# Kernel optimization log

Hardware: AMD Instinct MI355X
Metric: run time of the kernel (lower is better)

## Reference

```python
import jax, jax.numpy as jnp
import numpy as np

H = 8192   # lattice vertex count (all levels, synthetic, == hash_cnt)
N0 = 8192  # output point count
F = 15     # permutohedral filter size: (t+1)^(d+1) - t^(d+1), t=1, d=3
NEG = 0.1  # LeakyReLU negative slope

def lrelu(x):
    return jnp.where(x >= 0, x, NEG * x)

def conv1x1(x, w, b):
    # x (B,C,N), w (O,C), b (O,)
    return jnp.einsum('oc,bcn->bon', w, x) + b[None, :, None]

def splat(feat, bary, offset, num):
    # barycentric scatter of point features onto lattice: (B,C,N)->(B,C,num)
    w = feat[:, :, None, :] * bary[:, None, :, :]  # (B,C,4,N)
    def one(wb, ob):
        C = wb.shape[0]
        return jax.ops.segment_sum(wb.reshape(C, -1).T, ob.reshape(-1), num_segments=num).T
    return jax.vmap(one)(w, offset)

def gather(lat, idx):
    # lat (B,C,H), idx (B,K,N) -> (B,C,K,N)
    return jax.vmap(lambda f, i: f[:, i])(lat, idx)

def slice_lat(lat, bary, offset):
    # barycentric interpolation from lattice back to points: (B,C,N)
    return jnp.einsum('bcjn,bjn->bcn', gather(lat, offset), bary)

def blur_mlp(lat, nbrs, w0, b0, w1, b1):
    # BilateralConvFlex blur: gather F lattice neighbors, 1x1-conv MLP (last_relu=False)
    g = gather(lat, nbrs)  # (B,C,F,H)
    B, C, Fk, Hk = g.shape
    h = lrelu(conv1x1(g.reshape(B, C * Fk, Hk), w0, b0))
    return conv1x1(h, w1, b1)

def corr_block(feat1_pts, feat2_lat, prev_pts, bary1, off1, out_bary, out_off,
               idx1, idx2, wc0, bc0, wc1, bc1, wo0, bo0, wo1, bo1):
    # BilateralCorrelationFlex: splat pc1, hash-indexed patch correlation with pc2
    # lattice, per-displacement corr MLP, flatten over displacements, out MLP, slice.
    L1 = splat(feat1_pts, bary1, off1, H)                  # (B,C,H)
    x = gather(L1, idx1) * gather(feat2_lat, idx2)         # (B,C,F,H)
    if prev_pts is not None:
        P1 = splat(prev_pts, bary1, off1, H)
        x = jnp.concatenate([x, gather(P1, idx1)], axis=1)
    h = lrelu(jnp.einsum('oc,bcfh->bofh', wc0, x) + bc0[None, :, None, None])
    h = lrelu(jnp.einsum('oc,bcfh->bofh', wc1, h) + bc1[None, :, None, None])
    B, Co, Fk, Hk = h.shape
    h = lrelu(conv1x1(h.reshape(B, Co * Fk, Hk), wo0, bo0))
    h = conv1x1(h, wo1, bo1)                               # last_relu=False
    return slice_lat(h, out_bary, out_off)

def setup_inputs():
    key = jax.random.key(0)
    ks = iter(jax.random.split(key, 100))
    def randn(shape):
        return jax.random.normal(next(ks), shape, dtype=jnp.float32)
    def bary(n):
        b = jax.random.uniform(next(ks), (1, 4, n), dtype=jnp.float32)
        return b / jnp.sum(b, axis=1, keepdims=True)
    def ridx(shape, hi):
        return jax.random.randint(next(ks), shape, 0, hi)
    def W(o, c):
        return jax.random.normal(next(ks), (o, c), dtype=jnp.float32) / np.float32(np.sqrt(c))
    def bias(o):
        return jax.random.normal(next(ks), (o,), dtype=jnp.float32) * 0.01
    inp = {}
    for n in ['feat0_1', 'feat0_2', 'feat0_4', 'feat1_1', 'feat1_2', 'feat1_4']:
        inp[n] = randn((1, 32, H))
    for n in ['g2_pc1_el_minus_gr', 'g2_pc2_el_minus_gr', 'g1_pc1_el_minus_gr', 'g1_pc2_el_minus_gr']:
        inp[n] = randn((1, 4, H))
    inp['g2_pc1_barycentric'] = bary(H); inp['g2_pc2_barycentric'] = bary(H)
    inp['g1_pc1_barycentric'] = bary(H); inp['g1_pc2_barycentric'] = bary(H)
    inp['g0_pc1_barycentric'] = bary(N0)
    for n in ['g2_pc1_lattice_offset', 'g2_pc2_lattice_offset', 'g1_pc1_lattice_offset', 'g1_pc2_lattice_offset']:
        inp[n] = ridx((1, 4, H), H)
    inp['g0_pc1_lattice_offset'] = ridx((1, 4, N0), H)
    for n in ['g1_pc1_blur_neighbors', 'g1_pc2_blur_neighbors', 'g0_pc1_blur_neighbors', 'g0_pc2_blur_neighbors',
              'g1_pc1_corr_indices', 'g1_pc2_corr_indices', 'g0_pc1_corr_indices', 'g0_pc2_corr_indices']:
        inp[n] = ridx((1, F, H), H)
    inp['w_embed2'] = W(128, 32); inp['b_embed2'] = bias(128)
    inp['w_embed1'] = W(256, 32); inp['b_embed1'] = bias(256)
    inp['w_up2_0'] = W(256, 132 * F); inp['b_up2_0'] = bias(256)
    inp['w_up2_1'] = W(256, 256); inp['b_up2_1'] = bias(256)
    inp['w_up1_0'] = W(512, 516 * F); inp['b_up1_0'] = bias(512)
    inp['w_up1_1'] = W(512, 512); inp['b_up1_1'] = bias(512)
    inp['w_c2_corr0'] = W(32, 256); inp['b_c2_corr0'] = bias(32)
    inp['w_c2_corr1'] = W(32, 32); inp['b_c2_corr1'] = bias(32)
    inp['w_c2_out0'] = W(256, 32 * F); inp['b_c2_out0'] = bias(256)
    inp['w_c2_out1'] = W(256, 256); inp['b_c2_out1'] = bias(256)
    inp['w_c1_corr0'] = W(32, 512 + 256); inp['b_c1_corr0'] = bias(32)
    inp['w_c1_corr1'] = W(32, 32); inp['b_c1_corr1'] = bias(32)
    inp['w_c1_out0'] = W(512, 32 * F); inp['b_c1_out0'] = bias(512)
    inp['w_c1_out1'] = W(512, 512); inp['b_c1_out1'] = bias(512)
    inp['w_s4'] = W(512, 512); inp['b_s4'] = bias(512)
    inp['w_s2'] = W(256, 512); inp['b_s2'] = bias(256)
    inp['w_s1'] = W(3, 256); inp['b_s1'] = bias(3)
    return inp

def reference(feat0_1, feat0_2, feat0_4, feat1_1, feat1_2, feat1_4,
              g2_pc1_el_minus_gr, g2_pc2_el_minus_gr, g1_pc1_el_minus_gr, g1_pc2_el_minus_gr,
              g2_pc1_barycentric, g2_pc2_barycentric, g1_pc1_barycentric, g1_pc2_barycentric, g0_pc1_barycentric,
              g2_pc1_lattice_offset, g2_pc2_lattice_offset, g1_pc1_lattice_offset, g1_pc2_lattice_offset, g0_pc1_lattice_offset,
              g1_pc1_blur_neighbors, g1_pc2_blur_neighbors, g0_pc1_blur_neighbors, g0_pc2_blur_neighbors,
              g1_pc1_corr_indices, g1_pc2_corr_indices, g0_pc1_corr_indices, g0_pc2_corr_indices,
              w_embed2, b_embed2, w_embed1, b_embed1,
              w_up2_0, b_up2_0, w_up2_1, b_up2_1, w_up1_0, b_up1_0, w_up1_1, b_up1_1,
              w_c2_corr0, b_c2_corr0, w_c2_corr1, b_c2_corr1, w_c2_out0, b_c2_out0, w_c2_out1, b_c2_out1,
              w_c1_corr0, b_c1_corr0, w_c1_corr1, b_c1_corr1, w_c1_out0, b_c1_out0, w_c1_out1, b_c1_out1,
              w_s4, b_s4, w_s2, b_s2, w_s1, b_s1):
    # conv4_embed and feat*_4 are defined but unused in the original forward.
    f0_2 = lrelu(conv1x1(feat0_2, w_embed2, b_embed2))
    f1_2 = lrelu(conv1x1(feat1_2, w_embed2, b_embed2))
    blur0 = blur_mlp(jnp.concatenate([g2_pc1_el_minus_gr, f0_2], axis=1),
                     g1_pc1_blur_neighbors, w_up2_0, b_up2_0, w_up2_1, b_up2_1)
    pcl0_2 = slice_lat(blur0, g2_pc1_barycentric, g2_pc1_lattice_offset)
    pcl0_2_to_1 = slice_lat(blur0, g1_pc1_barycentric, g1_pc1_lattice_offset)
    blur1 = blur_mlp(jnp.concatenate([g2_pc2_el_minus_gr, f1_2], axis=1),
                     g1_pc2_blur_neighbors, w_up2_0, b_up2_0, w_up2_1, b_up2_1)
    pcl1_2 = slice_lat(blur1, g2_pc2_barycentric, g2_pc2_lattice_offset)
    pcl1_2_to_1 = slice_lat(blur1, g1_pc2_barycentric, g1_pc2_lattice_offset)
    corr2 = corr_block(pcl0_2, pcl1_2, None, g2_pc1_barycentric, g2_pc1_lattice_offset,
                       g1_pc1_barycentric, g1_pc1_lattice_offset,
                       g1_pc1_corr_indices, g1_pc2_corr_indices,
                       w_c2_corr0, b_c2_corr0, w_c2_corr1, b_c2_corr1,
                       w_c2_out0, b_c2_out0, w_c2_out1, b_c2_out1)
    f0_1 = lrelu(conv1x1(feat0_1, w_embed1, b_embed1))
    f1_1 = lrelu(conv1x1(feat1_1, w_embed1, b_embed1))
    lat0 = blur_mlp(jnp.concatenate([g1_pc1_el_minus_gr, pcl0_2_to_1, f0_1], axis=1),
                    g0_pc1_blur_neighbors, w_up1_0, b_up1_0, w_up1_1, b_up1_1)
    pcl0_1 = slice_lat(lat0, g1_pc1_barycentric, g1_pc1_lattice_offset)
    lat1 = blur_mlp(jnp.concatenate([g1_pc2_el_minus_gr, pcl1_2_to_1, f1_1], axis=1),
                    g0_pc2_blur_neighbors, w_up1_0, b_up1_0, w_up1_1, b_up1_1)
    pcl1_1 = slice_lat(lat1, g1_pc2_barycentric, g1_pc2_lattice_offset)
    corr1 = corr_block(pcl0_1, pcl1_1, corr2, g1_pc1_barycentric, g1_pc1_lattice_offset,
                       g0_pc1_barycentric, g0_pc1_lattice_offset,
                       g0_pc1_corr_indices, g0_pc2_corr_indices,
                       w_c1_corr0, b_c1_corr0, w_c1_corr1, b_c1_corr1,
                       w_c1_out0, b_c1_out0, w_c1_out1, b_c1_out1)
    res = lrelu(conv1x1(corr1, w_s4, b_s4))
    res = lrelu(conv1x1(res, w_s2, b_s2))
    return conv1x1(res, w_s1, b_s1)  # (1, 3, N0)
```

## Files before the change

kernel.cpp:

```cpp
#include <hip/hip_runtime.h>
#include <hip/hip_bf16.h>

#define HDIM 8192
#define FK 15

typedef __attribute__((ext_vector_type(8))) short bf16x8;
typedef __attribute__((ext_vector_type(4))) float f32x4;

__device__ __forceinline__ void gload_lds16(const void* g, void* l) {
    __builtin_amdgcn_global_load_lds(
        (const __attribute__((address_space(1))) void*)g,
        (__attribute__((address_space(3))) void*)l, 16, 0, 0);
}

__global__ void k_pack(const float* __restrict__ W, __hip_bfloat16* __restrict__ P,
                       int O, int C, int Cp, int Fk, int mode) {
    int e = blockIdx.x * 256 + threadIdx.x;
    int total = Fk * Cp * O;
    if (e >= total) return;
    int j = e & 7;
    int lane = (e >> 3) & 63;
    int tile = e >> 9;
    int OT = O >> 4;
    int ot = tile % OT, kt = tile / OT;
    int o = ot * 16 + (lane & 15);
    int kk = kt * 32 + (lane >> 4) * 8 + j;
    float v;
    if (mode == 1) {
        int f = kk / Cp, c = kk % Cp;
        v = (c < C) ? W[(size_t)o * C * Fk + (size_t)c * Fk + f] : 0.f;
    } else if (mode == 2) {
        int f = kk >> 5, oo = kk & 31;
        v = W[(size_t)o * 480 + oo * 15 + f];
    } else {
        v = W[(size_t)o * C + kk];
    }
    P[e] = __float2bfloat16(v);
}

__global__ void k_copy_el(const float* __restrict__ el, __hip_bfloat16* __restrict__ catT,
                          int N, int ld) {
    int n = blockIdx.x * 256 + threadIdx.x;
    if (n >= N) return;
#pragma unroll
    for (int j = 0; j < 4; ++j)
        catT[(size_t)n * ld + j] = __float2bfloat16(el[(size_t)j * N + n]);
}

__global__ __launch_bounds__(256) void k_embed(const float* __restrict__ X,
                                               const float* __restrict__ W,
                                               const float* __restrict__ b,
                                               __hip_bfloat16* __restrict__ outT,
                                               int N, int O, int ld, int coff) {
    __shared__ float Xs[32][65];
    int tid = threadIdx.x;
    int n0 = blockIdx.x * 64;
    for (int e = tid; e < 32 * 64; e += 256) {
        int nn = e & 63, c = e >> 6;
        Xs[c][nn] = X[(size_t)c * N + n0 + nn];
    }
    __syncthreads();
    int ol = tid & 63, nl = tid >> 6;
    for (int o0 = 0; o0 < O; o0 += 64) {
        int o = o0 + ol;
        float wv[32];
#pragma unroll
        for (int c = 0; c < 32; ++c) wv[c] = W[o * 32 + c];
        float bv = b[o];
        for (int nn = nl; nn < 64; nn += 4) {
            float acc = bv;
#pragma unroll
            for (int c = 0; c < 32; ++c) acc += wv[c] * Xs[c][nn];
            acc = acc >= 0.f ? acc : 0.1f * acc;
            outT[(size_t)(n0 + nn) * ld + coff + o] = __float2bfloat16(acc);
        }
    }
}

struct W4 { bf16x8 r0, r1, r2, r3; };

template<int OG, int HG, int MR>
__global__ __launch_bounds__(512, 2) void k_blur_fat(
    const __hip_bfloat16* __restrict__ A0b, const __hip_bfloat16* __restrict__ A1b,
    const int* __restrict__ n0, const int* __restrict__ n1,
    const __hip_bfloat16* __restrict__ Wb, float* __restrict__ hbuf,
    int Cp, int O, int H) {
    __shared__ short abuf[3 * 4096];
    __shared__ int idx_s[8 * 128];
    int z = blockIdx.z;
    int strm = z >> 1, kh = z & 1;
    const unsigned short* A = (const unsigned short*)(strm ? A1b : A0b);
    const int* nbrs = strm ? n1 : n0;
    int CpT = Cp >> 5, OT = O >> 4;
    int fbeg = kh ? 8 : 0;
    int fcnt = kh ? (FK - 8) : 8;
    int S = fcnt * CpT;
    float* outp = hbuf + (size_t)z * ((size_t)H * (size_t)O);
    const unsigned short* Wp = (const unsigned short*)Wb;
    int tid = threadIdx.x, lane = tid & 63, wid = tid >> 6;
    int r16 = lane & 15, g = lane >> 4;
    int og = (OG == 8) ? wid : (wid & 3);
    int hg = (OG == 8) ? 0 : (wid >> 2);
    int h0 = blockIdx.x * 128;
    int srow = tid >> 2;
    int sgseg = (tid & 3) ^ ((tid >> 3) & 3);
    int pseg = g ^ ((r16 >> 1) & 3);
    int hgbase = hg * (MR * 16);
    char* abase = (char*)abuf;

    for (int e = tid; e < fcnt * 128; e += 512)
        idx_s[e] = nbrs[(size_t)(fbeg + (e >> 7)) * H + h0 + (e & 127)];
    __syncthreads();

    f32x4 acc[MR][4];
#pragma unroll
    for (int m = 0; m < MR; ++m)
#pragma unroll
        for (int n = 0; n < 4; ++n) acc[m][n] = (f32x4){0.f, 0.f, 0.f, 0.f};

    W4 wA, wB, wC;
    int tS = 0, cS = 0, fS = 0;

#define STAGE_AW(SLOTA, W)                                                         \
    do {                                                                           \
        int gi = idx_s[fS * 128 + srow];                                           \
        gload_lds16(A + (size_t)gi * Cp + cS * 32 + sgseg * 8,                     \
                    abase + (SLOTA) * 8192 + wid * 1024);                          \
        const unsigned short* wbp =                                                \
            Wp + ((size_t)(((fbeg + fS) * CpT + cS) * OT + og * 4)) * 512 + lane * 8; \
        W.r0 = *(const bf16x8*)(wbp);                                              \
        W.r1 = *(const bf16x8*)(wbp + 512);                                        \
        W.r2 = *(const bf16x8*)(wbp + 1024);                                       \
        W.r3 = *(const bf16x8*)(wbp + 1536);                                       \
        if (tS < S - 1) { ++tS; if (++cS == CpT) { cS = 0; ++fS; } }               \
    } while (0)

#define FITER(SLOT, WCUR, WNXT)                                                    \
    do {                                                                           \
        __builtin_amdgcn_sched_barrier(0);                                         \
        asm volatile("s_waitcnt vmcnt(5)" ::: "memory");                           \
        __builtin_amdgcn_sched_barrier(0);                                         \
        __builtin_amdgcn_s_barrier();                                              \
        __builtin_amdgcn_sched_barrier(0);                                         \
        STAGE_AW(((SLOT) + 2) % 3, WNXT);                                          \
        const short* ab = abuf + (SLOT) * 4096;                                    \
        bf16x8 av[MR];                                                             \
        _Pragma("unroll")                                                          \
        for (int rb = 0; rb < MR; ++rb)                                            \
            av[rb] = *(const bf16x8*)(ab + (hgbase + rb * 16 + r16) * 32 + pseg * 8); \
        _Pragma("unroll")                                                          \
        for (int rb = 0; rb < MR; ++rb) {                                          \
            acc[rb][0] = __builtin_amdgcn_mfma_f32_16x16x32_bf16(av[rb], WCUR.r0, acc[rb][0], 0, 0, 0); \
            acc[rb][1] = __builtin_amdgcn_mfma_f32_16x16x32_bf16(av[rb], WCUR.r1, acc[rb][1], 0, 0, 0); \
            acc[rb][2] = __builtin_amdgcn_mfma_f32_16x16x32_bf16(av[rb], WCUR.r2, acc[rb][2], 0, 0, 0); \
            acc[rb][3] = __builtin_amdgcn_mfma_f32_16x16x32_bf16(av[rb], WCUR.r3, acc[rb][3], 0, 0, 0); \
        }                                                                          \
    } while (0)

    STAGE_AW(0, wA);
    STAGE_AW(1, wB);
    for (int t = 0; t < S; t += 3) {
        FITER(0, wA, wC);
        if (t + 1 < S) FITER(1, wB, wA);
        if (t + 2 < S) FITER(2, wC, wB);
    }
#undef FITER
#undef STAGE_AW

#pragma unroll
    for (int n = 0; n < 4; ++n) {
        int o = og * 64 + n * 16 + r16;
#pragma unroll
        for (int m = 0; m < MR; ++m)
#pragma unroll
            for (int i = 0; i < 4; ++i)
                outp[(size_t)(h0 + hgbase + m * 16 + g * 4 + i) * O + o] = acc[m][n][i];
    }
}

__global__ void k_comb(const float* __restrict__ p, const float* __restrict__ bias,
                       __hip_bfloat16* __restrict__ out, int NO, int Om) {
    int i = blockIdx.x * 256 + threadIdx.x;
    int stride = gridDim.x * 256;
    for (; i < NO; i += stride) {
        float v = p[i] + p[i + NO] + bias[i & Om];
        v = v >= 0.f ? v : 0.1f * v;
        out[i] = __float2bfloat16(v);
    }
}

#define DEF_PIPE_VARS                                                              \
    bf16x8 a00, a01, w00, w01, w02, w03;                                           \
    bf16x8 a10, a11, w10, w11, w12, w13;                                           \
    bf16x8 a20, a21, w20, w21, w22, w23;

#define LOADST(J, TEND, FEND)                                                      \
    do {                                                                           \
        const unsigned short* a0p = A + (size_t)i0c * Cp + cL * 32 + g * 8;        \
        const unsigned short* a1p = A + (size_t)i1c * Cp + cL * 32 + g * 8;        \
        a##J##0 = *(const bf16x8*)a0p;                                             \
        a##J##1 = *(const bf16x8*)a1p;                                             \
        const unsigned short* wbp = Wp + ((size_t)(tL * OT + otb)) * 512 + lane * 8; \
        w##J##0 = *(const bf16x8*)(wbp);                                           \
        w##J##1 = *(const bf16x8*)(wbp + 512);                                     \
        w##J##2 = *(const bf16x8*)(wbp + 1024);                                    \
        w##J##3 = *(const bf16x8*)(wbp + 1536);                                    \
        if (tL < (TEND) - 1) {                                                     \
            ++tL;                                                                  \
            if (++cL == CpT) {                                                     \
                cL = 0; ++fL;                                                      \
                i0c = i0n; i1c = i1n;                                              \
                if (fL + 1 < (FEND)) {                                             \
                    i0n = nbrs ? nbrs[(size_t)(fL + 1) * H + hrow] : hrow;         \
                    i1n = nbrs ? nbrs[(size_t)(fL + 1) * H + hrow + 16] : (hrow + 16); \
                }                                                                  \
            }                                                                      \
        }                                                                          \
    } while (0)

#define MFMAST(J)                                                                  \
    do {                                                                           \
        acc[0][0] = __builtin_amdgcn_mfma_f32_16x16x32_bf16(a##J##0, w##J##0, acc[0][0], 0, 0, 0); \
        acc[0][1] = __builtin_amdgcn_mfma_f32_16x16x32_bf16(a##J##0, w##J##1, acc[0][1], 0, 0, 0); \
        acc[0][2] = __builtin_amdgcn_mfma_f32_16x16x32_bf16(a##J##0, w##J##2, acc[0][2], 0, 0, 0); \
        acc[0][3] = __builtin_amdgcn_mfma_f32_16x16x32_bf16(a##J##0, w##J##3, acc[0][3], 0, 0, 0); \
        acc[1][0] = __builtin_amdgcn_mfma_f32_16x16x32_bf16(a##J##1, w##J##0, acc[1][0], 0, 0, 0); \
        acc[1][1] = __builtin_amdgcn_mfma_f32_16x16x32_bf16(a##J##1, w##J##1, acc[1][1], 0, 0, 0); \
        acc[1][2] = __builtin_amdgcn_mfma_f32_16x16x32_bf16(a##J##1, w##J##2, acc[1][2], 0, 0, 0); \
        acc[1][3] = __builtin_amdgcn_mfma_f32_16x16x32_bf16(a##J##1, w##J##3, acc[1][3], 0, 0, 0); \
    } while (0)

__global__ __launch_bounds__(256) void k_mfma_gemm(const __hip_bfloat16* __restrict__ Ab,
                                                   const int* __restrict__ nbrs,
                                                   const __hip_bfloat16* __restrict__ Wb,
                                                   const float* __restrict__ bias,
                                                   float* __restrict__ outF,
                                                   __hip_bfloat16* __restrict__ outB,
                                                   int Cp, int Fk, int O, int H, int act,
                                                   const __hip_bfloat16* Ab1,
                                                   float* outF1, __hip_bfloat16* outB1) {
    if (blockIdx.z) { Ab = Ab1; outF = outF1; outB = outB1; }
    const unsigned short* A = (const unsigned short*)Ab;
    const unsigned short* Wp = (const unsigned short*)Wb;
    int tid = threadIdx.x, lane = tid & 63, w = tid >> 6;
    int r16 = lane & 15, g = lane >> 4;
    int h0 = blockIdx.x * 128, o0 = blockIdx.y * 64;
    int OT = O >> 4, CpT = Cp >> 5, S = Fk * CpT;
    int otb = o0 >> 4;
    int w32 = w * 32;
    int hrow = h0 + w32 + r16;

    int i0c = nbrs ? nbrs[hrow] : hrow;
    int i1c = nbrs ? nbrs[hrow + 16] : (hrow + 16);
    int i0n = i0c, i1n = i1c;
    if (Fk > 1) {
        i0n = nbrs[(size_t)H + hrow];
        i1n = nbrs[(size_t)H + hrow + 16];
    }

    f32x4 acc[2][4];
#pragma unroll
    for (int m = 0; m < 2; ++m)
#pragma unroll
        for (int n = 0; n < 4; ++n) acc[m][n] = (f32x4){0.f, 0.f, 0.f, 0.f};

    DEF_PIPE_VARS
    int tL = 0, cL = 0, fL = 0;

    LOADST(0, S, Fk);
    LOADST(1, S, Fk);
    for (int sb = 0; sb < S; sb += 3) {
        LOADST(2, S, Fk);
        MFMAST(0);
        LOADST(0, S, Fk);
        if (sb + 1 < S) MFMAST(1);
        LOADST(1, S, Fk);
        if (sb + 2 < S) MFMAST(2);
    }

#pragma unroll
    for (int n = 0; n < 4; ++n) {
        int o = o0 + n * 16 + r16;
        float bv = bias[o];
#pragma unroll
        for (int m = 0; m < 2; ++m) {
#pragma unroll
            for (int i = 0; i < 4; ++i) {
                int h = h0 + w32 + m * 16 + g * 4 + i;
                float v = acc[m][n][i] + bv;
                if (act) v = v >= 0.f ? v : 0.1f * v;
                if (outF) outF[(size_t)h * O + o] = v;
                if (outB) outB[(size_t)h * O + o] = __float2bfloat16(v);
            }
        }
    }
}

__global__ void k_slice(const float* __restrict__ latT, const float* __restrict__ bary,
                        const int* __restrict__ off, float* __restrict__ outT,
                        int N, int C, int ld, int coff) {
    int cl = threadIdx.x & 63, rr = threadIdx.x >> 6;
    int n = blockIdx.x * 4 + rr;
    int c = blockIdx.y * 64 + cl;
    float s = 0.f;
#pragma unroll
    for (int j = 0; j < 4; ++j) {
        int o = off[(size_t)j * N + n];
        float w = bary[(size_t)j * N + n];
        s += latT[(size_t)o * C + c] * w;
    }
    outT[(size_t)n * ld + coff + c] = s;
}

__global__ void k_slice_b(const float* __restrict__ latT, const float* __restrict__ bary,
                          const int* __restrict__ off, __hip_bfloat16* __restrict__ outT,
                          int N, int C, int ld, int coff) {
    int cl = threadIdx.x & 63, rr = threadIdx.x >> 6;
    int n = blockIdx.x * 4 + rr;
    int c = blockIdx.y * 64 + cl;
    float s = 0.f;
#pragma unroll
    for (int j = 0; j < 4; ++j) {
        int o = off[(size_t)j * N + n];
        float w = bary[(size_t)j * N + n];
        s += latT[(size_t)o * C + c] * w;
    }
    outT[(size_t)n * ld + coff + c] = __float2bfloat16(s);
}

__global__ void k_splat(const float* __restrict__ featT, const float* __restrict__ bary,
                        const int* __restrict__ off, float* __restrict__ latT,
                        int N, int C) {
    int cl = threadIdx.x & 63, rr = threadIdx.x >> 6;
    int n = blockIdx.x * 4 + rr;
    int c = blockIdx.y * 64 + cl;
    float v = featT[(size_t)n * C + c];
#pragma unroll
    for (int j = 0; j < 4; ++j) {
        int o = off[(size_t)j * N + n];
        float w = bary[(size_t)j * N + n];
        atomicAdd(&latT[(size_t)o * C + c], v * w);
    }
}

__global__ __launch_bounds__(256) void k_corr_mfma(const float* __restrict__ L1T,
                                                   const float* __restrict__ f2T,
                                                   const float* __restrict__ P1T,
                                                   const int* __restrict__ idx1,
                                                   const int* __restrict__ idx2,
                                                   const __hip_bfloat16* __restrict__ W0p,
                                                   const float* __restrict__ b0,
                                                   const __hip_bfloat16* __restrict__ W1p,
                                                   const float* __restrict__ b1,
                                                   __hip_bfloat16* __restrict__ h1T,
                                                   int H, int C1, int C2) {
    __shared__ __hip_bfloat16 As[64 * 72];
    __shared__ __hip_bfloat16 A0s[64 * 40];
    __shared__ int i1s[64], i2s[64];
    int tid = threadIdx.x;
    int p0 = blockIdx.x * 64;
    int f = p0 >> 13;
    int h0 = p0 & (HDIM - 1);
    if (tid < 64) {
        i1s[tid] = idx1[(size_t)f * H + h0 + tid];
        i2s[tid] = idx2[(size_t)f * H + h0 + tid];
    }
    __syncthreads();
    int lane = tid & 63, wid = tid >> 6;
    int wh = wid * 16;
    int r16 = lane & 15, g = lane >> 4;
    int srow = tid >> 2, sseg = tid & 3;
    int K = C1 + C2;
    const unsigned short* W0u = (const unsigned short*)W0p;
    const unsigned short* W1u = (const unsigned short*)W1p;
    f32x4 acc[2];
    acc[0] = (f32x4){0.f, 0.f, 0.f, 0.f};
    acc[1] = (f32x4){0.f, 0.f, 0.f, 0.f};

    for (int c0 = 0; c0 < K; c0 += 64) {
        int cb = c0 + sseg * 16;
        float x[16];
        if (cb < C1) {
            const float4* a4 = (const float4*)(L1T + (size_t)i1s[srow] * C1 + cb);
            const float4* b4 = (const float4*)(f2T + (size_t)i2s[srow] * C1 + cb);
#pragma unroll
            for (int q = 0; q < 4; ++q) {
                float4 av = a4[q], bv = b4[q];
                x[q * 4 + 0] = av.x * bv.x; x[q * 4 + 1] = av.y * bv.y;
                x[q * 4 + 2] = av.z * bv.z; x[q * 4 + 3] = av.w * bv.w;
            }
        } else {
            const float4* a4 = (const float4*)(P1T + (size_t)i1s[srow] * C2 + (cb - C1));
#pragma unroll
            for (int q = 0; q < 4; ++q) {
                float4 av = a4[q];
                x[q * 4 + 0] = av.x; x[q * 4 + 1] = av.y;
                x[q * 4 + 2] = av.z; x[q * 4 + 3] = av.w;
            }
        }
        __syncthreads();
        __hip_bfloat16* dst = &As[srow * 72 + sseg * 16];
#pragma unroll
        for (int q = 0; q < 16; ++q) dst[q] = __float2bfloat16(x[q]);
        __syncthreads();
        int ktg = c0 >> 5;
#pragma unroll
        for (int kt = 0; kt < 2; ++kt) {
            bf16x8 a = *(const bf16x8*)(&As[(wh + r16) * 72 + kt * 32 + g * 8]);
            const unsigned short* wb = W0u + (size_t)((ktg + kt) * 2) * 512 + lane * 8;
            bf16x8 bf0 = *(const bf16x8*)(wb);
            bf16x8 bf1 = *(const bf16x8*)(wb + 512);
            acc[0] = __builtin_amdgcn_mfma_f32_16x16x32_bf16(a, bf0, acc[0], 0, 0, 0);
            acc[1] = __builtin_amdgcn_mfma_f32_16x16x32_bf16(a, bf1, acc[1], 0, 0, 0);
        }
    }
    __syncthreads();
#pragma unroll
    for (int ot = 0; ot < 2; ++ot) {
        int o = ot * 16 + r16;
        float bv = b0[o];
#pragma unroll
        for (int i = 0; i < 4; ++i) {
            int pr = wh + g * 4 + i;
            float v = acc[ot][i] + bv;
            v = v >= 0.f ? v : 0.1f * v;
            A0s[pr * 40 + o] = __float2bfloat16(v);
        }
    }
    __syncthreads();
    bf16x8 a1 = *(const bf16x8*)(&A0s[(wh + r16) * 40 + g * 8]);
    bf16x8 w1f0 = *(const bf16x8*)(W1u + lane * 8);
    bf16x8 w1f1 = *(const bf16x8*)(W1u + 512 + lane * 8);
    f32x4 acc1[2];
    acc1[0] = (f32x4){0.f, 0.f, 0.f, 0.f};
    acc1[1] = (f32x4){0.f, 0.f, 0.f, 0.f};
    acc1[0] = __builtin_amdgcn_mfma_f32_16x16x32_bf16(a1, w1f0, acc1[0], 0, 0, 0);
    acc1[1] = __builtin_amdgcn_mfma_f32_16x16x32_bf16(a1, w1f1, acc1[1], 0, 0, 0);
#pragma unroll
    for (int ot = 0; ot < 2; ++ot) {
        int o = ot * 16 + r16;
        float bv = b1[o];
#pragma unroll
        for (int i = 0; i < 4; ++i) {
            int h = h0 + wh + g * 4 + i;
            float v = acc1[ot][i] + bv;
            v = v >= 0.f ? v : 0.1f * v;
            h1T[(size_t)h * 480 + f * 32 + o] = __float2bfloat16(v);
        }
    }
}

__global__ void k_final(const float* __restrict__ r2T, const float* __restrict__ W,
                        const float* __restrict__ b, float* __restrict__ out, int N) {
    int n = blockIdx.x * 256 + threadIdx.x;
    if (n >= N) return;
    float s0 = b[0], s1 = b[1], s2 = b[2];
    const float4* x4 = (const float4*)(r2T + (size_t)n * 256);
    for (int q = 0; q < 64; ++q) {
        float4 v = x4[q];
        float xs[4] = {v.x, v.y, v.z, v.w};
#pragma unroll
        for (int u = 0; u < 4; ++u) {
            int c = 4 * q + u;
            s0 = fmaf(W[c], xs[u], s0);
            s1 = fmaf(W[256 + c], xs[u], s1);
            s2 = fmaf(W[512 + c], xs[u], s2);
        }
    }
    out[n] = s0;
    out[(size_t)N + n] = s1;
    out[(size_t)2 * N + n] = s2;
}

extern "C" void kernel_launch(void* const* d_in, const int* in_sizes, int n_in,
                              void* d_out, int out_size, void* d_ws, size_t ws_size,
                              hipStream_t stream) {
    const int N = HDIM;
    auto F32 = [&](int i) { return (const float*)d_in[i]; };
    auto I32 = [&](int i) { return (const int*)d_in[i]; };

    char* base = (char*)d_ws;
    size_t off = 0;
    auto allocB = [&](size_t elems) -> __hip_bfloat16* {
        __hip_bfloat16* r = (__hip_bfloat16*)(base + off);
        off += ((elems * 2 + 255) / 256) * 256;
        return r;
    };
    auto allocF = [&](size_t elems) -> float* {
        float* r = (float*)(base + off);
        off += ((elems * 4 + 255) / 256) * 256;
        return r;
    };

    __hip_bfloat16* pw_up2   = allocB((size_t)15 * 160 * 256);
    __hip_bfloat16* pw_up1   = allocB((size_t)15 * 544 * 512);
    __hip_bfloat16* pw_up2_1 = allocB((size_t)256 * 256);
    __hip_bfloat16* pw_up1_1 = allocB((size_t)512 * 512);
    __hip_bfloat16* pw_c2o   = allocB((size_t)480 * 256);
    __hip_bfloat16* pw_c2o1  = allocB((size_t)256 * 256);
    __hip_bfloat16* pw_c1o   = allocB((size_t)480 * 512);
    __hip_bfloat16* pw_c1o1  = allocB((size_t)512 * 512);
    __hip_bfloat16* pw_s4    = allocB((size_t)512 * 512);
    __hip_bfloat16* pw_s2    = allocB((size_t)512 * 256);
    __hip_bfloat16* pw_cc20  = allocB((size_t)256 * 32);
    __hip_bfloat16* pw_cc21  = allocB((size_t)32 * 32);
    __hip_bfloat16* pw_cc10  = allocB((size_t)768 * 32);
    __hip_bfloat16* pw_cc11  = allocB((size_t)32 * 32);
    __hip_bfloat16* catb2a = allocB((size_t)N * 160);
    __hip_bfloat16* catb2b = allocB((size_t)N * 160);
    __hip_bfloat16* catb1a = allocB((size_t)N * 544);
    __hip_bfloat16* catb1b = allocB((size_t)N * 544);
    __hip_bfloat16* ab512a = allocB((size_t)N * 512);
    __hip_bfloat16* ab512b = allocB((size_t)N * 512);
    __hip_bfloat16* ab256a = allocB((size_t)N * 256);
    __hip_bfloat16* ab256b = allocB((size_t)N * 256);
    __hip_bfloat16* h1b    = allocB((size_t)N * 480);
    __hip_bfloat16* corr1b = allocB((size_t)N * 512);
    float* T512a  = allocF((size_t)N * 512);
    float* T512b  = allocF((size_t)N * 512);
    float* pcl512 = allocF((size_t)N * 512);
    float* pcl01  = allocF((size_t)N * 512);
    float* pcl11  = allocF((size_t)N * 512);
    float* SL256  = allocF((size_t)N * 256);
    float* corr2T = allocF((size_t)N * 256);
    float* hbuf   = allocF((size_t)4 * N * 512);
    float* pclA = pcl512;
    float* pclB = pcl512 + (size_t)N * 256;
    float* SL512 = pcl512;
    float* SP256 = SL256;
    (void)ws_size; (void)in_sizes; (void)n_in; (void)out_size;

    auto pack = [&](const float* W, __hip_bfloat16* P, int O, int C, int Cp, int Fk, int mode) {
        int total = Fk * Cp * O;
        k_pack<<<(total + 255) / 256, 256, 0, stream>>>(W, P, O, C, Cp, Fk, mode);
    };
    pack(F32(32), pw_up2,   256, 132, 160, 15, 1);
    pack(F32(36), pw_up1,   512, 516, 544, 15, 1);
    pack(F32(34), pw_up2_1, 256, 256, 256, 1, 0);
    pack(F32(38), pw_up1_1, 512, 512, 512, 1, 0);
    pack(F32(44), pw_c2o,   256, 480, 480, 1, 2);
    pack(F32(46), pw_c2o1,  256, 256, 256, 1, 0);
    pack(F32(52), pw_c1o,   512, 480, 480, 1, 2);
    pack(F32(54), pw_c1o1,  512, 512, 512, 1, 0);
    pack(F32(56), pw_s4,    512, 512, 512, 1, 0);
    pack(F32(58), pw_s2,    256, 512, 512, 1, 0);
    pack(F32(40), pw_cc20,  32, 256, 256, 1, 0);
    pack(F32(42), pw_cc21,  32, 32, 32, 1, 0);
    pack(F32(48), pw_cc10,  32, 768, 768, 1, 0);
    pack(F32(50), pw_cc11,  32, 32, 32, 1, 0);

    hipMemsetAsync(catb2a, 0, (size_t)N * 160 * 2, stream);
    hipMemsetAsync(catb2b, 0, (size_t)N * 160 * 2, stream);
    hipMemsetAsync(catb1a, 0, (size_t)N * 544 * 2, stream);
    hipMemsetAsync(catb1b, 0, (size_t)N * 544 * 2, stream);
    hipMemsetAsync(SL256,  0, (size_t)N * 256 * 4, stream);

    k_copy_el<<<32, 256, 0, stream>>>(F32(6), catb2a, N, 160);
    k_embed<<<128, 256, 0, stream>>>(F32(1), F32(28), F32(29), catb2a, N, 128, 160, 4);
    k_copy_el<<<32, 256, 0, stream>>>(F32(7), catb2b, N, 160);
    k_embed<<<128, 256, 0, stream>>>(F32(4), F32(28), F32(29), catb2b, N, 128, 160, 4);
    k_blur_fat<4, 2, 4><<<dim3(64, 1, 4), 512, 0, stream>>>(catb2a, catb2b, I32(20), I32(21),
                                                            pw_up2, hbuf, 160, 256, N);
    k_comb<<<2048, 256, 0, stream>>>(hbuf, F32(33), ab256a, N * 256, 255);
    k_comb<<<2048, 256, 0, stream>>>(hbuf + (size_t)2 * N * 256, F32(33), ab256b, N * 256, 255);
    k_mfma_gemm<<<dim3(64, 4, 2), 256, 0, stream>>>(ab256a, nullptr, pw_up2_1, F32(35),
                                                    T512a, nullptr, 256, 1, 256, N, 0,
                                                    ab256b, T512b, nullptr);
    k_slice<<<dim3(2048, 4), 256, 0, stream>>>(T512a, F32(10), I32(15), pclA, N, 256, 256, 0);
    k_slice_b<<<dim3(2048, 4), 256, 0, stream>>>(T512a, F32(12), I32(17), catb1a, N, 256, 544, 4);
    k_slice<<<dim3(2048, 4), 256, 0, stream>>>(T512b, F32(11), I32(16), pclB, N, 256, 256, 0);
    k_slice_b<<<dim3(2048, 4), 256, 0, stream>>>(T512b, F32(13), I32(18), catb1b, N, 256, 544, 4);

    k_splat<<<dim3(2048, 4), 256, 0, stream>>>(pclA, F32(10), I32(15), SL256, N, 256);
    k_corr_mfma<<<FK * HDIM / 64, 256, 0, stream>>>(SL256, pclB, (const float*)nullptr,
                                                    I32(24), I32(25), pw_cc20, F32(41),
                                                    pw_cc21, F32(43), h1b, N, 256, 0);
    k_mfma_gemm<<<dim3(64, 4), 256, 0, stream>>>(h1b, nullptr, pw_c2o, F32(45),
                                                 nullptr, ab256a, 480, 1, 256, N, 1,
                                                 nullptr, nullptr, nullptr);
    k_mfma_gemm<<<dim3(64, 4), 256, 0, stream>>>(ab256a, nullptr, pw_c2o1, F32(47),
                                                 T512a, nullptr, 256, 1, 256, N, 0,
                                                 nullptr, nullptr, nullptr);
    k_slice<<<dim3(2048, 4), 256, 0, stream>>>(T512a, F32(12), I32(17), corr2T, N, 256, 256, 0);

    k_copy_el<<<32, 256, 0, stream>>>(F32(8), catb1a, N, 544);
    k_embed<<<128, 256, 0, stream>>>(F32(0), F32(30), F32(31), catb1a, N, 256, 544, 260);
    k_copy_el<<<32, 256, 0, stream>>>(F32(9), catb1b, N, 544);
    k_embed<<<128, 256, 0, stream>>>(F32(3), F32(30), F32(31), catb1b, N, 256, 544, 260);
    k_blur_fat<8, 1, 8><<<dim3(64, 1, 4), 512, 0, stream>>>(catb1a, catb1b, I32(22), I32(23),
                                                            pw_up1, hbuf, 544, 512, N);
    k_comb<<<2048, 256, 0, stream>>>(hbuf, F32(37), ab512a, N * 512, 511);
    k_comb<<<2048, 256, 0, stream>>>(hbuf + (size_t)2 * N * 512, F32(37), ab512b, N * 512, 511);
    k_mfma_gemm<<<dim3(64, 8, 2), 256, 0, stream>>>(ab512a, nullptr, pw_up1_1, F32(39),
                                                    T512a, nullptr, 512, 1, 512, N, 0,
                                                    ab512b, T512b, nullptr);
    k_slice<<<dim3(2048, 8), 256, 0, stream>>>(T512a, F32(12), I32(17), pcl01, N, 512, 512, 0);
    k_slice<<<dim3(2048, 8), 256, 0, stream>>>(T512b, F32(13), I32(18), pcl11, N, 512, 512, 0);

    hipMemsetAsync(SL512, 0, (size_t)N * 512 * 4, stream);
    k_splat<<<dim3(2048, 8), 256, 0, stream>>>(pcl01, F32(12), I32(17), SL512, N, 512);
    hipMemsetAsync(SP256, 0, (size_t)N * 256 * 4, stream);
    k_splat<<<dim3(2048, 4), 256, 0, stream>>>(corr2T, F32(12), I32(17), SP256, N, 256);
    k_corr_mfma<<<FK * HDIM / 64, 256, 0, stream>>>(SL512, pcl11, SP256,
                                                    I32(26), I32(27), pw_cc10, F32(49),
                                                    pw_cc11, F32(51), h1b, N, 512, 256);
    k_mfma_gemm<<<dim3(64, 8), 256, 0, stream>>>(h1b, nullptr, pw_c1o, F32(53),
                                                 nullptr, ab512a, 480, 1, 512, N, 1,
                                                 nullptr, nullptr, nullptr);
    k_mfma_gemm<<<dim3(64, 8), 256, 0, stream>>>(ab512a, nullptr, pw_c1o1, F32(55),
                                                 T512a, nullptr, 512, 1, 512, N, 0,
                                                 nullptr, nullptr, nullptr);
    k_slice_b<<<dim3(2048, 8), 256, 0, stream>>>(T512a, F32(14), I32(19), corr1b, N, 512, 512, 0);

    k_mfma_gemm<<<dim3(64, 8), 256, 0, stream>>>(corr1b, nullptr, pw_s4, F32(57),
                                                 nullptr, ab512a, 512, 1, 512, N, 1,
                                                 nullptr, nullptr, nullptr);
    k_mfma_gemm<<<dim3(64, 4), 256, 0, stream>>>(ab512a, nullptr, pw_s2, F32(59),
                                                 T512a, nullptr, 512, 1, 256, N, 1,
                                                 nullptr, nullptr, nullptr);
    k_final<<<32, 256, 0, stream>>>(T512a, F32(60), F32(61), (float*)d_out, N);
}
```

Measured before the change: 818.5 us.

## Use bf16 gather sources in corr, retile blur over output groups, merge launches

The correlation kernel now gathers bf16 copies of the splatted lattice, the pc2 features and the previous-level features instead of fp32. This halves the bytes read in its random-access gather, at the cost of extra conversion kernels and lower precision. The blur kernel is retiled to 256 rows per block, with the output channels split across blockIdx.y and two gathered loads issued per thread. The paired copy_el and embed launches for the two point clouds are merged into single launches using blockIdx.z.

After: 708.9 us. 13.4% less time.

```diff
diff --git a/kernel.cpp b/kernel.cpp
--- a/kernel.cpp
+++ b/kernel.cpp
@@ -5,12 +5,20 @@
 #define FK 15
 
 typedef __attribute__((ext_vector_type(8))) short bf16x8;
+typedef __attribute__((ext_vector_type(8))) unsigned short u16x8;
 typedef __attribute__((ext_vector_type(4))) float f32x4;
 
 __device__ __forceinline__ void gload_lds16(const void* g, void* l) {
     __builtin_amdgcn_global_load_lds(
         (const __attribute__((address_space(1))) void*)g,
         (__attribute__((address_space(3))) void*)l, 16, 0, 0);
+}
+
+__device__ __forceinline__ float b2f(unsigned short s) {
+    unsigned u = (unsigned)s << 16;
+    float f;
+    __builtin_memcpy(&f, &u, 4);
+    return f;
 }
 
 __global__ void k_pack(const float* __restrict__ W, __hip_bfloat16* __restrict__ P,
@@ -38,8 +46,11 @@
     P[e] = __float2bfloat16(v);
 }
 
-__global__ void k_copy_el(const float* __restrict__ el, __hip_bfloat16* __restrict__ catT,
-                          int N, int ld) {
+__global__ void k_copy_el2(const float* __restrict__ el0, const float* __restrict__ el1,
+                           __hip_bfloat16* __restrict__ c0, __hip_bfloat16* __restrict__ c1,
+                           int N, int ld) {
+    const float* el = blockIdx.z ? el1 : el0;
+    __hip_bfloat16* catT = blockIdx.z ? c1 : c0;
     int n = blockIdx.x * 256 + threadIdx.x;
     if (n >= N) return;
 #pragma unroll
@@ -47,11 +58,15 @@
         catT[(size_t)n * ld + j] = __float2bfloat16(el[(size_t)j * N + n]);
 }
 
-__global__ __launch_bounds__(256) void k_embed(const float* __restrict__ X,
-                                               const float* __restrict__ W,
-                                               const float* __restrict__ b,
-                                               __hip_bfloat16* __restrict__ outT,
-                                               int N, int O, int ld, int coff) {
+__global__ __launch_bounds__(256) void k_embed2(const float* __restrict__ X0,
+                                                const float* __restrict__ X1,
+                                                const float* __restrict__ W,
+                                                const float* __restrict__ b,
+                                                __hip_bfloat16* __restrict__ o0,
+                                                __hip_bfloat16* __restrict__ o1,
+                                                int N, int O, int ld, int coff) {
+    const float* X = blockIdx.z ? X1 : X0;
+    __hip_bfloat16* outT = blockIdx.z ? o1 : o0;
     __shared__ float Xs[32][65];
     int tid = threadIdx.x;
     int n0 = blockIdx.x * 64;
@@ -61,8 +76,8 @@
     }
     __syncthreads();
     int ol = tid & 63, nl = tid >> 6;
-    for (int o0 = 0; o0 < O; o0 += 64) {
-        int o = o0 + ol;
+    for (int o0i = 0; o0i < O; o0i += 64) {
+        int o = o0i + ol;
         float wv[32];
 #pragma unroll
         for (int c = 0; c < 32; ++c) wv[c] = W[o * 32 + c];
@@ -77,16 +92,26 @@
     }
 }
 
+__global__ void k_cvt(const float* __restrict__ in, __hip_bfloat16* __restrict__ out, int n) {
+    int i = (blockIdx.x * 256 + threadIdx.x) * 4;
+    if (i >= n) return;
+    float4 v = *(const float4*)(in + i);
+    out[i + 0] = __float2bfloat16(v.x);
+    out[i + 1] = __float2bfloat16(v.y);
+    out[i + 2] = __float2bfloat16(v.z);
+    out[i + 3] = __float2bfloat16(v.w);
+}
+
 struct W4 { bf16x8 r0, r1, r2, r3; };
 
 template<int OG, int HG, int MR>
-__global__ __launch_bounds__(512, 2) void k_blur_fat(
+__global__ __launch_bounds__(512, 2) void k_blur_f3(
     const __hip_bfloat16* __restrict__ A0b, const __hip_bfloat16* __restrict__ A1b,
     const int* __restrict__ n0, const int* __restrict__ n1,
     const __hip_bfloat16* __restrict__ Wb, float* __restrict__ hbuf,
     int Cp, int O, int H) {
-    __shared__ short abuf[3 * 4096];
-    __shared__ int idx_s[8 * 128];
+    __shared__ short abuf[3 * 8192];
+    __shared__ int idx_s[8 * 256];
     int z = blockIdx.z;
     int strm = z >> 1, kh = z & 1;
     const unsigned short* A = (const unsigned short*)(strm ? A1b : A0b);
@@ -95,21 +120,24 @@
     int fbeg = kh ? 8 : 0;
     int fcnt = kh ? (FK - 8) : 8;
     int S = fcnt * CpT;
-    float* outp = hbuf + (size_t)z * ((size_t)H * (size_t)O);
+    size_t NO = (size_t)H * O;
+    float* outp = hbuf + (size_t)z * NO;
     const unsigned short* Wp = (const unsigned short*)Wb;
     int tid = threadIdx.x, lane = tid & 63, wid = tid >> 6;
     int r16 = lane & 15, g = lane >> 4;
-    int og = (OG == 8) ? wid : (wid & 3);
-    int hg = (OG == 8) ? 0 : (wid >> 2);
-    int h0 = blockIdx.x * 128;
-    int srow = tid >> 2;
-    int sgseg = (tid & 3) ^ ((tid >> 3) & 3);
+    int og = wid % OG;
+    int hg = wid / OG;
+    int h0 = blockIdx.x * 256;
+    int obase = blockIdx.y * (OG * 64);
+    int otb = blockIdx.y * (OG * 4);
+    int srw = lane >> 2;
+    int sgseg = (lane & 3) ^ ((lane >> 3) & 3);
     int pseg = g ^ ((r16 >> 1) & 3);
     int hgbase = hg * (MR * 16);
     char* abase = (char*)abuf;
 
-    for (int e = tid; e < fcnt * 128; e += 512)
-        idx_s[e] = nbrs[(size_t)(fbeg + (e >> 7)) * H + h0 + (e & 127)];
+    for (int e = tid; e < fcnt * 256; e += 512)
+        idx_s[e] = nbrs[(size_t)(fbeg + (e >> 8)) * H + h0 + (e & 255)];
     __syncthreads();
 
     f32x4 acc[MR][4];
@@ -123,11 +151,14 @@
 
 #define STAGE_AW(SLOTA, W)                                                         \
     do {                                                                           \
-        int gi = idx_s[fS * 128 + srow];                                           \
-        gload_lds16(A + (size_t)gi * Cp + cS * 32 + sgseg * 8,                     \
-                    abase + (SLOTA) * 8192 + wid * 1024);                          \
+        int gi0 = idx_s[fS * 256 + wid * 16 + srw];                                \
+        int gi1 = idx_s[fS * 256 + (wid + 8) * 16 + srw];                          \
+        gload_lds16(A + (size_t)gi0 * Cp + cS * 32 + sgseg * 8,                    \
+                    abase + (SLOTA) * 16384 + wid * 1024);                         \
+        gload_lds16(A + (size_t)gi1 * Cp + cS * 32 + sgseg * 8,                    \
+                    abase + (SLOTA) * 16384 + (wid + 8) * 1024);                   \
         const unsigned short* wbp =                                                \
-            Wp + ((size_t)(((fbeg + fS) * CpT + cS) * OT + og * 4)) * 512 + lane * 8; \
+            Wp + ((size_t)(((fbeg + fS) * CpT + cS) * OT + otb + og * 4)) * 512 + lane * 8; \
         W.r0 = *(const bf16x8*)(wbp);                                              \
         W.r1 = *(const bf16x8*)(wbp + 512);                                        \
         W.r2 = *(const bf16x8*)(wbp + 1024);                                       \
@@ -138,12 +169,12 @@
 #define FITER(SLOT, WCUR, WNXT)                                                    \
     do {                                                                           \
         __builtin_amdgcn_sched_barrier(0);                                         \
-        asm volatile("s_waitcnt vmcnt(5)" ::: "memory");                           \
+        asm volatile("s_waitcnt vmcnt(6)" ::: "memory");                           \
         __builtin_amdgcn_sched_barrier(0);                                         \
         __builtin_amdgcn_s_barrier();                                              \
         __builtin_amdgcn_sched_barrier(0);                                         \
         STAGE_AW(((SLOT) + 2) % 3, WNXT);                                          \
-        const short* ab = abuf + (SLOT) * 4096;                                    \
+        const short* ab = abuf + (SLOT) * 8192;                                    \
         bf16x8 av[MR];                                                             \
         _Pragma("unroll")                                                          \
         for (int rb = 0; rb < MR; ++rb)                                            \
@@ -169,7 +200,7 @@
 
 #pragma unroll
     for (int n = 0; n < 4; ++n) {
-        int o = og * 64 + n * 16 + r16;
+        int o = obase + og * 64 + n * 16 + r16;
 #pragma unroll
         for (int m = 0; m < MR; ++m)
 #pragma unroll
@@ -343,9 +374,9 @@
     }
 }
 
-__global__ __launch_bounds__(256) void k_corr_mfma(const float* __restrict__ L1T,
-                                                   const float* __restrict__ f2T,
-                                                   const float* __restrict__ P1T,
+__global__ __launch_bounds__(256) void k_corr_mfma(const __hip_bfloat16* __restrict__ L1b,
+                                                   const __hip_bfloat16* __restrict__ f2b,
+                                                   const __hip_bfloat16* __restrict__ P1b,
                                                    const int* __restrict__ idx1,
                                                    const int* __restrict__ idx2,
                                                    const __hip_bfloat16* __restrict__ W0p,
@@ -357,6 +388,9 @@
     __shared__ __hip_bfloat16 As[64 * 72];
     __shared__ __hip_bfloat16 A0s[64 * 40];
     __shared__ int i1s[64], i2s[64];
+    const unsigned short* L1u = (const unsigned short*)L1b;
+    const unsigned short* f2u = (const unsigned short*)f2b;
+    const unsigned short* P1u = (const unsigned short*)P1b;
     int tid = threadIdx.x;
     int p0 = blockIdx.x * 64;
     int f = p0 >> 13;
@@ -381,21 +415,22 @@
         int cb = c0 + sseg * 16;
         float x[16];
         if (cb < C1) {
-            const float4* a4 = (const float4*)(L1T + (size_t)i1s[srow] * C1 + cb);
-            const float4* b4 = (const float4*)(f2T + (size_t)i2s[srow] * C1 + cb);
-#pragma unroll
-            for (int q = 0; q < 4; ++q) {
-                float4 av = a4[q], bv = b4[q];
-                x[q * 4 + 0] = av.x * bv.x; x[q * 4 + 1] = av.y * bv.y;
-                x[q * 4 + 2] = av.z * bv.z; x[q * 4 + 3] = av.w * bv.w;
+            u16x8 av0 = *(const u16x8*)(L1u + (size_t)i1s[srow] * C1 + cb);
+            u16x8 av1 = *(const u16x8*)(L1u + (size_t)i1s[srow] * C1 + cb + 8);
+            u16x8 bv0 = *(const u16x8*)(f2u + (size_t)i2s[srow] * C1 + cb);
+            u16x8 bv1 = *(const u16x8*)(f2u + (size_t)i2s[srow] * C1 + cb + 8);
+#pragma unroll
+            for (int u = 0; u < 8; ++u) {
+                x[u]     = b2f(av0[u]) * b2f(bv0[u]);
+                x[8 + u] = b2f(av1[u]) * b2f(bv1[u]);
             }
         } else {
-            const float4* a4 = (const float4*)(P1T + (size_t)i1s[srow] * C2 + (cb - C1));
-#pragma unroll
-            for (int q = 0; q < 4; ++q) {
-                float4 av = a4[q];
-                x[q * 4 + 0] = av.x; x[q * 4 + 1] = av.y;
-                x[q * 4 + 2] = av.z; x[q * 4 + 3] = av.w;
+            u16x8 p0v = *(const u16x8*)(P1u + (size_t)i1s[srow] * C2 + (cb - C1));
+            u16x8 p1v = *(const u16x8*)(P1u + (size_t)i1s[srow] * C2 + (cb - C1) + 8);
+#pragma unroll
+            for (int u = 0; u < 8; ++u) {
+                x[u] = b2f(p0v[u]);
+                x[8 + u] = b2f(p1v[u]);
             }
         }
         __syncthreads();
@@ -516,16 +551,19 @@
     __hip_bfloat16* ab256b = allocB((size_t)N * 256);
     __hip_bfloat16* h1b    = allocB((size_t)N * 480);
     __hip_bfloat16* corr1b = allocB((size_t)N * 512);
+    __hip_bfloat16* SL256b = allocB((size_t)N * 256);
+    __hip_bfloat16* SL512b = allocB((size_t)N * 512);
+    __hip_bfloat16* SP256b = allocB((size_t)N * 256);
+    __hip_bfloat16* pclBb  = allocB((size_t)N * 256);
+    __hip_bfloat16* pcl11b = allocB((size_t)N * 512);
     float* T512a  = allocF((size_t)N * 512);
     float* T512b  = allocF((size_t)N * 512);
     float* pcl512 = allocF((size_t)N * 512);
     float* pcl01  = allocF((size_t)N * 512);
-    float* pcl11  = allocF((size_t)N * 512);
     float* SL256  = allocF((size_t)N * 256);
     float* corr2T = allocF((size_t)N * 256);
     float* hbuf   = allocF((size_t)4 * N * 512);
     float* pclA = pcl512;
-    float* pclB = pcl512 + (size_t)N * 256;
     float* SL512 = pcl512;
     float* SP256 = SL256;
     (void)ws_size; (void)in_sizes; (void)n_in; (void)out_size;
@@ -555,12 +593,11 @@
     hipMemsetAsync(catb1b, 0, (size_t)N * 544 * 2, stream);
     hipMemsetAsync(SL256,  0, (size_t)N * 256 * 4, stream);
 
-    k_copy_el<<<32, 256, 0, stream>>>(F32(6), catb2a, N, 160);
-    k_embed<<<128, 256, 0, stream>>>(F32(1), F32(28), F32(29), catb2a, N, 128, 160, 4);
-    k_copy_el<<<32, 256, 0, stream>>>(F32(7), catb2b, N, 160);
-    k_embed<<<128, 256, 0, stream>>>(F32(4), F32(28), F32(29), catb2b, N, 128, 160, 4);
-    k_blur_fat<4, 2, 4><<<dim3(64, 1, 4), 512, 0, stream>>>(catb2a, catb2b, I32(20), I32(21),
-                                                            pw_up2, hbuf, 160, 256, N);
+    k_copy_el2<<<dim3(32, 1, 2), 256, 0, stream>>>(F32(6), F32(7), catb2a, catb2b, N, 160);
+    k_embed2<<<dim3(128, 1, 2), 256, 0, stream>>>(F32(1), F32(4), F32(28), F32(29),
+                                                  catb2a, catb2b, N, 128, 160, 4);
+    k_blur_f3<2, 4, 4><<<dim3(32, 2, 4), 512, 0, stream>>>(catb2a, catb2b, I32(20), I32(21),
+                                                           pw_up2, hbuf, 160, 256, N);
     k_comb<<<2048, 256, 0, stream>>>(hbuf, F32(33), ab256a, N * 256, 255);
     k_comb<<<2048, 256, 0, stream>>>(hbuf + (size_t)2 * N * 256, F32(33), ab256b, N * 256, 255);
     k_mfma_gemm<<<dim3(64, 4, 2), 256, 0, stream>>>(ab256a, nullptr, pw_up2_1, F32(35),
@@ -568,11 +605,12 @@
                                                     ab256b, T512b, nullptr);
     k_slice<<<dim3(2048, 4), 256, 0, stream>>>(T512a, F32(10), I32(15), pclA, N, 256, 256, 0);
     k_slice_b<<<dim3(2048, 4), 256, 0, stream>>>(T512a, F32(12), I32(17), catb1a, N, 256, 544, 4);
-    k_slice<<<dim3(2048, 4), 256, 0, stream>>>(T512b, F32(11), I32(16), pclB, N, 256, 256, 0);
+    k_slice_b<<<dim3(2048, 4), 256, 0, stream>>>(T512b, F32(11), I32(16), pclBb, N, 256, 256, 0);
     k_slice_b<<<dim3(2048, 4), 256, 0, stream>>>(T512b, F32(13), I32(18), catb1b, N, 256, 544, 4);
 
     k_splat<<<dim3(2048, 4), 256, 0, stream>>>(pclA, F32(10), I32(15), SL256, N, 256);
-    k_corr_mfma<<<FK * HDIM / 64, 256, 0, stream>>>(SL256, pclB, (const float*)nullptr,
+    k_cvt<<<(N * 256 / 4 + 255) / 256, 256, 0, stream>>>(SL256, SL256b, N * 256);
+    k_corr_mfma<<<FK * HDIM / 64, 256, 0, stream>>>(SL256b, pclBb, (const __hip_bfloat16*)nullptr,
                                                     I32(24), I32(25), pw_cc20, F32(41),
                                                     pw_cc21, F32(43), h1b, N, 256, 0);
     k_mfma_gemm<<<dim3(64, 4), 256, 0, stream>>>(h1b, nullptr, pw_c2o, F32(45),
@@ -583,25 +621,26 @@
                                                  nullptr, nullptr, nullptr);
     k_slice<<<dim3(2048, 4), 256, 0, stream>>>(T512a, F32(12), I32(17), corr2T, N, 256, 256, 0);
 
-    k_copy_el<<<32, 256, 0, stream>>>(F32(8), catb1a, N, 544);
-    k_embed<<<128, 256, 0, stream>>>(F32(0), F32(30), F32(31), catb1a, N, 256, 544, 260);
-    k_copy_el<<<32, 256, 0, stream>>>(F32(9), catb1b, N, 544);
-    k_embed<<<128, 256, 0, stream>>>(F32(3), F32(30), F32(31), catb1b, N, 256, 544, 260);
-    k_blur_fat<8, 1, 8><<<dim3(64, 1, 4), 512, 0, stream>>>(catb1a, catb1b, I32(22), I32(23),
-                                                            pw_up1, hbuf, 544, 512, N);
+    k_copy_el2<<<dim3(32, 1, 2), 256, 0, stream>>>(F32(8), F32(9), catb1a, catb1b, N, 544);
+    k_embed2<<<dim3(128, 1, 2), 256, 0, stream>>>(F32(0), F32(3), F32(30), F32(31),
+                                                  catb1a, catb1b, N, 256, 544, 260);
+    k_blur_f3<4, 2, 8><<<dim3(32, 2, 4), 512, 0, stream>>>(catb1a, catb1b, I32(22), I32(23),
+                                                           pw_up1, hbuf, 544, 512, N);
     k_comb<<<2048, 256, 0, stream>>>(hbuf, F32(37), ab512a, N * 512, 511);
     k_comb<<<2048, 256, 0, stream>>>(hbuf + (size_t)2 * N * 512, F32(37), ab512b, N * 512, 511);
     k_mfma_gemm<<<dim3(64, 8, 2), 256, 0, stream>>>(ab512a, nullptr, pw_up1_1, F32(39),
                                                     T512a, nullptr, 512, 1, 512, N, 0,
                                                     ab512b, T512b, nullptr);
     k_slice<<<dim3(2048, 8), 256, 0, stream>>>(T512a, F32(12), I32(17), pcl01, N, 512, 512, 0);
-    k_slice<<<dim3(2048, 8), 256, 0, stream>>>(T512b, F32(13), I32(18), pcl11, N, 512, 512, 0);
+    k_slice_b<<<dim3(2048, 8), 256, 0, stream>>>(T512b, F32(13), I32(18), pcl11b, N, 512, 512, 0);
 
     hipMemsetAsync(SL512, 0, (size_t)N * 512 * 4, stream);
     k_splat<<<dim3(2048, 8), 256, 0, stream>>>(pcl01, F32(12), I32(17), SL512, N, 512);
     hipMemsetAsync(SP256, 0, (size_t)N * 256 * 4, stream);
     k_splat<<<dim3(2048, 4), 256, 0, stream>>>(corr2T, F32(12), I32(17), SP256, N, 256);
-    k_corr_mfma<<<FK * HDIM / 64, 256, 0, stream>>>(SL512, pcl11, SP256,
+    k_cvt<<<(N * 512 / 4 + 255) / 256, 256, 0, stream>>>(SL512, SL512b, N * 512);
+    k_cvt<<<(N * 256 / 4 + 255) / 256, 256, 0, stream>>>(SP256, SP256b, N * 256);
+    k_corr_mfma<<<FK * HDIM / 64, 256, 0, stream>>>(SL512b, pcl11b, SP256b,
                                                     I32(26), I32(27), pw_cc10, F32(49),
                                                     pw_cc11, F32(51), h1b, N, 512, 256);
     k_mfma_gemm<<<dim3(64, 8), 256, 0, stream>>>(h1b, nullptr, pw_c1o, F32(53),
```
